# Performance work log

Hardware: AMD Instinct MI355X
Metric: run time of the kernel (lower is better)

Reference implementation:

```python
import jax, jax.numpy as jnp
import numpy as np

DIM_IN = 1024
DIM_OUT = 1024
BATCH = 4
SEQ = 2048


def setup_inputs() -> dict:
    key = jax.random.key(0)
    kx, kq, kk, kv = jax.random.split(key, 4)
    scale = 1.0 / np.sqrt(DIM_IN)
    x = jax.random.normal(kx, (BATCH, SEQ, DIM_IN), dtype=jnp.float32)
    # Weights stored as [dim_in, dim_out] (transpose of torch Linear's [out, in]);
    # y = x @ W is equivalent math to torch's x @ W_t.T
    Wq = jax.random.normal(kq, (DIM_IN, DIM_OUT), dtype=jnp.float32) * scale
    Wk = jax.random.normal(kk, (DIM_IN, DIM_OUT), dtype=jnp.float32) * scale
    Wv = jax.random.normal(kv, (DIM_IN, DIM_OUT), dtype=jnp.float32) * scale
    return {"x": x, "Wq": Wq, "Wk": Wk, "Wv": Wv}


def reference(x, Wq, Wk, Wv):
    # x: [b, s, d_in]; single-head causal self-attention (dropout=0 -> identity)
    q = jnp.einsum("bsd,de->bse", x, Wq)
    k = jnp.einsum("bsd,de->bse", x, Wk)
    v = jnp.einsum("bsd,de->bse", x, Wv)
    dim_k = k.shape[-1]
    scores = jnp.einsum("bqe,bke->bqk", q, k) / jnp.sqrt(jnp.float32(dim_k))
    s = x.shape[1]
    causal = jnp.tril(jnp.ones((s, s), dtype=bool))  # True = keep
    scores = jnp.where(causal[None, :, :], scores, -jnp.inf)
    weights = jax.nn.softmax(scores, axis=-1)
    context = jnp.einsum("bqk,bke->bqe", weights, v)
    return context
```

## Files before the change

kernel.cpp:

```cpp
#include <hip/hip_runtime.h>
#include <cstdint>
#include <cstddef>

typedef unsigned short u16;
typedef __bf16 bf16x8 __attribute__((ext_vector_type(8)));
typedef float f32x4 __attribute__((ext_vector_type(4)));

__device__ inline u16 f2b(float f) {
    uint32_t u = __builtin_bit_cast(uint32_t, f);
    u += 0x7FFFu + ((u >> 16) & 1u);
    return (u16)(u >> 16);
}

__device__ inline void gl2lds16(const u16* g, u16* l) {
    __builtin_amdgcn_global_load_lds(
        (const __attribute__((address_space(1))) void*)g,
        (__attribute__((address_space(3))) void*)l, 16, 0, 0);
}

__global__ void prep_kernel(const float* __restrict__ x, u16* __restrict__ xb,
                            const float* __restrict__ Wq,
                            const float* __restrict__ Wk,
                            const float* __restrict__ Wv,
                            u16* __restrict__ QKWT, u16* __restrict__ WvT) {
    __shared__ u16 t[32][33];
    const int bid = blockIdx.x;
    if (bid < 8192) {
        size_t i = ((size_t)bid * 256 + threadIdx.x) * 4;
        float4 v = *(const float4*)(x + i);
        uint2 pack;
        pack.x = (uint32_t)f2b(v.x) | ((uint32_t)f2b(v.y) << 16);
        pack.y = (uint32_t)f2b(v.z) | ((uint32_t)f2b(v.w) << 16);
        *(uint2*)(xb + i) = pack;
        return;
    }
    const int tb = bid - 8192;
    const int z = tb >> 10;
    const int rem = tb & 1023;
    const int by = (rem >> 5) * 32;
    const int bx = (rem & 31) * 32;
    const float* W = (z == 0) ? Wq : ((z == 1) ? Wk : Wv);
    u16* dst = (z == 0) ? QKWT : ((z == 1) ? QKWT + 1024 * 1024 : WvT);
    const float scale = (z == 0) ? 0.03125f : 1.0f;
    const int tx = threadIdx.x & 31, ty = threadIdx.x >> 5;
    #pragma unroll
    for (int r = 0; r < 32; r += 8)
        t[ty + r][tx] = f2b(W[(size_t)(by + ty + r) * 1024 + bx + tx] * scale);
    __syncthreads();
    #pragma unroll
    for (int r = 0; r < 32; r += 8)
        dst[(size_t)(bx + ty + r) * 1024 + (by + tx)] = t[tx][ty + r];
}

template<int EPI>
__device__ __forceinline__ void gemm_body(
    u16* __restrict__ smem,
    const u16* __restrict__ A, int lda,
    const u16* __restrict__ B, int ldb,
    char* __restrict__ Cb, int ldc,
    int m0, int n0, int Kloc, float* __restrict__ lrow, bool split = false) {
    constexpr int BK = 32;
    const int tid = threadIdx.x;
    const int lane = tid & 63, wave = tid >> 6;
    const int wm = wave >> 1, wn = wave & 1;
    const int fl = lane & 15, fh = lane >> 4;

    const int q0 = wave * 2;
    const int srow = lane >> 2;
    const int skoff = ((lane & 3) ^ ((lane >> 3) & 3)) * 8;
    const u16* ApL0 = A + (size_t)(m0 + q0 * 16 + srow) * lda + skoff;
    const u16* ApL1 = ApL0 + (size_t)16 * lda;
    const u16* BpL0 = B + (size_t)(n0 + q0 * 16 + srow) * ldb + skoff;
    const u16* BpL1 = BpL0 + (size_t)16 * ldb;

    u16* const Ab[2] = { smem, smem + 4096 };
    u16* const Bb[2] = { smem + 8192, smem + 12288 };

    auto issue = [&](int buf, int k0) {
        gl2lds16(ApL0 + k0, Ab[buf] + q0 * 512);
        gl2lds16(ApL1 + k0, Ab[buf] + q0 * 512 + 512);
        gl2lds16(BpL0 + k0, Bb[buf] + q0 * 512);
        gl2lds16(BpL1 + k0, Bb[buf] + q0 * 512 + 512);
    };

    const f32x4 vzero = {0.f, 0.f, 0.f, 0.f};
    f32x4 acc[4][4];
    #pragma unroll
    for (int i = 0; i < 4; ++i)
        #pragma unroll
        for (int j = 0; j < 4; ++j) acc[i][j] = vzero;

    const int rcx = (fl >> 1) & 3;

    issue(0, 0);
    int buf = 0;
    for (int k0 = 0; k0 < Kloc; k0 += BK, buf ^= 1) {
        __syncthreads();
        if (k0 + BK < Kloc) issue(buf ^ 1, k0 + BK);
        bf16x8 af[4], bfr[4];
        #pragma unroll
        for (int t = 0; t < 4; ++t) {
            af[t]  = *(const bf16x8*)&Ab[buf][(wm * 64 + t * 16 + fl) * BK + (fh ^ rcx) * 8];
            bfr[t] = *(const bf16x8*)&Bb[buf][(wn * 64 + t * 16 + fl) * BK + (fh ^ rcx) * 8];
        }
        #pragma unroll
        for (int mt = 0; mt < 4; ++mt)
            #pragma unroll
            for (int nt = 0; nt < 4; ++nt)
                acc[mt][nt] = __builtin_amdgcn_mfma_f32_16x16x32_bf16(
                    af[mt], bfr[nt], acc[mt][nt], 0, 0, 0);
    }

    if (EPI == 0) {
        u16* Cp = (u16*)Cb;
        #pragma unroll
        for (int mt = 0; mt < 4; ++mt)
            #pragma unroll
            for (int nt = 0; nt < 4; ++nt)
                #pragma unroll
                for (int r = 0; r < 4; ++r) {
                    int row = m0 + wm * 64 + mt * 16 + fh * 4 + r;
                    int col = n0 + wn * 64 + nt * 16 + fl;
                    Cp[(size_t)row * ldc + col] = f2b(acc[mt][nt][r]);
                }
    } else if (EPI == 2) {
        u16* Cp = (u16*)Cb;
        #pragma unroll
        for (int mt = 0; mt < 4; ++mt)
            #pragma unroll
            for (int r = 0; r < 4; ++r) {
                int row = m0 + wm * 64 + mt * 16 + fh * 4 + r;
                float part = 0.f;
                #pragma unroll
                for (int nt = 0; nt < 4; ++nt) {
                    int col = n0 + wn * 64 + nt * 16 + fl;
                    float p = (col <= row) ? __expf(acc[mt][nt][r]) : 0.f;
                    part += p;
                    Cp[(size_t)row * ldc + col] = f2b(p);
                }
                #pragma unroll
                for (int off = 1; off < 16; off <<= 1)
                    part += __shfl_xor(part, off, 64);
                if (fl == 0) atomicAdd(lrow + row, part);
            }
    } else {
        float* Cp = (float*)Cb;
        #pragma unroll
        for (int mt = 0; mt < 4; ++mt)
            #pragma unroll
            for (int r = 0; r < 4; ++r) {
                int row = m0 + wm * 64 + mt * 16 + fh * 4 + r;
                float inv = 1.0f / lrow[row];
                #pragma unroll
                for (int nt = 0; nt < 4; ++nt) {
                    int col = n0 + wn * 64 + nt * 16 + fl;
                    float v = acc[mt][nt][r] * inv;
                    if (split) atomicAdd(&Cp[(size_t)row * ldc + col], v);
                    else       Cp[(size_t)row * ldc + col] = v;
                }
            }
    }
}

__global__ __launch_bounds__(256)
void proj_kernel(const u16* __restrict__ xb, const u16* __restrict__ QKWT,
                 const u16* __restrict__ WvT, u16* __restrict__ QK,
                 u16* __restrict__ Vt) {
    __shared__ __align__(16) u16 smem[16384];
    int bid = blockIdx.x;
    if (bid < 1024) {
        int jt = bid & 15, it = bid >> 4;
        gemm_body<0>(smem, xb, 1024, QKWT, 1024, (char*)QK, 2048,
                     it * 128, jt * 128, 1024, nullptr);
    } else {
        int b = bid - 1024;
        int jt = b & 63, it = b >> 6;
        gemm_body<0>(smem, WvT, 1024, xb, 1024, (char*)Vt, 8192,
                     it * 128, jt * 128, 1024, nullptr);
    }
}

__global__ __launch_bounds__(256)
void scores_kernel(const u16* __restrict__ QK, u16* __restrict__ P,
                   float* __restrict__ l) {
    __shared__ __align__(16) u16 smem[16384];
    const int t = blockIdx.x, z = blockIdx.y;
    int it = (int)((sqrtf(8.0f * t + 1.0f) - 1.0f) * 0.5f);
    while ((it + 1) * (it + 2) / 2 <= t) ++it;
    while (it * (it + 1) / 2 > t) --it;
    const int jt = t - it * (it + 1) / 2;
    const u16* Qz = QK + (size_t)z * 2048 * 2048;
    const u16* Kz = Qz + 1024;
    u16* Pz = P + (size_t)z * 2048 * 2048;
    gemm_body<2>(smem, Qz, 2048, Kz, 2048, (char*)Pz, 2048,
                 it * 128, jt * 128, 1024, l + (size_t)z * 2048);
}

__global__ __launch_bounds__(256)
void out_kernel(const u16* __restrict__ P, const u16* __restrict__ Vt,
                float* __restrict__ out, float* __restrict__ l) {
    __shared__ __align__(16) u16 smem[16384];
    const int jt = blockIdx.x, c = blockIdx.y, z = blockIdx.z;
    int it, k0, kloc;
    bool split;
    if (c < 16) {
        it = 8 + (c >> 1);
        kloc = (it + 1) * 64;
        k0 = (c & 1) * kloc;
        split = true;
    } else {
        it = c - 16;
        k0 = 0;
        kloc = (it + 1) * 128;
        split = false;
    }
    gemm_body<3>(smem, P + (size_t)z * 2048 * 2048 + k0, 2048,
                 Vt + (size_t)z * 2048 + k0, 8192,
                 (char*)(out + (size_t)z * 2048 * 1024), 1024,
                 it * 128, jt * 128, kloc, l + (size_t)z * 2048, split);
}

extern "C" void kernel_launch(void* const* d_in, const int* in_sizes, int n_in,
                              void* d_out, int out_size, void* d_ws, size_t ws_size,
                              hipStream_t stream) {
    (void)in_sizes; (void)n_in; (void)ws_size;
    const float* x  = (const float*)d_in[0];
    const float* Wq = (const float*)d_in[1];
    const float* Wk = (const float*)d_in[2];
    const float* Wv = (const float*)d_in[3];
    float* out = (float*)d_out;

    const size_t MB = 1u << 20;
    char* ws = (char*)d_ws;
    u16* xb   = (u16*)(ws);
    u16* QKWT = (u16*)(ws + 16 * MB);
    u16* WvT  = (u16*)(ws + 20 * MB);
    u16* QK   = (u16*)(ws + 22 * MB);
    u16* Vt   = (u16*)(ws + 54 * MB);
    u16* P    = (u16*)(ws + 70 * MB);
    float* l  = (float*)(ws + 102 * MB);

    hipMemsetAsync(l, 0, 8192 * sizeof(float), stream);
    hipMemsetAsync(out, 0, (size_t)out_size * sizeof(float), stream);
    prep_kernel<<<8192 + 3072, 256, 0, stream>>>(x, xb, Wq, Wk, Wv, QKWT, WvT);

    proj_kernel<<<1536, 256, 0, stream>>>(xb, QKWT, WvT, QK, Vt);
    scores_kernel<<<dim3(136, 4), 256, 0, stream>>>(QK, P, l);
    out_kernel<<<dim3(8, 24, 4), 256, 0, stream>>>(P, Vt, out, l);
}
```

Measured before the change: 266.1 us.

## Fuse memsets into prep kernel, rebalance causal split-K, drop LDS swizzle

Zeroing of the output and the row-sum buffer moves into extra work in prep_kernel, which removes two memset launches. The P·V kernel is re-partitioned into uniform 512-wide K chunks per causal row tile, giving 40 chunks per column tile, and batch is folded into the x grid dimension to even out work across blocks. The XOR swizzle on LDS tile addressing is removed, which simplifies the index math but may reintroduce LDS bank conflicts in the MFMA fragment loads. More blocks now take the atomic split path.

After: 289.7 us. +8.9%, slower.

```diff
diff --git a/kernel.cpp b/kernel.cpp
--- a/kernel.cpp
+++ b/kernel.cpp
@@ -22,7 +22,8 @@
                             const float* __restrict__ Wq,
                             const float* __restrict__ Wk,
                             const float* __restrict__ Wv,
-                            u16* __restrict__ QKWT, u16* __restrict__ WvT) {
+                            u16* __restrict__ QKWT, u16* __restrict__ WvT,
+                            float* __restrict__ out, float* __restrict__ l) {
     __shared__ u16 t[32][33];
     const int bid = blockIdx.x;
     if (bid < 8192) {
@@ -32,6 +33,12 @@
         pack.x = (uint32_t)f2b(v.x) | ((uint32_t)f2b(v.y) << 16);
         pack.y = (uint32_t)f2b(v.z) | ((uint32_t)f2b(v.w) << 16);
         *(uint2*)(xb + i) = pack;
+        *(float4*)(out + i) = make_float4(0.f, 0.f, 0.f, 0.f);
+        return;
+    }
+    if (bid >= 11264) {
+        size_t i = ((size_t)(bid - 11264) * 256 + threadIdx.x) * 4;
+        *(float4*)(l + i) = make_float4(0.f, 0.f, 0.f, 0.f);
         return;
     }
     const int tb = bid - 8192;
@@ -66,8 +73,7 @@
     const int fl = lane & 15, fh = lane >> 4;
 
     const int q0 = wave * 2;
-    const int srow = lane >> 2;
-    const int skoff = ((lane & 3) ^ ((lane >> 3) & 3)) * 8;
+    const int srow = lane >> 2, skoff = (lane & 3) * 8;
     const u16* ApL0 = A + (size_t)(m0 + q0 * 16 + srow) * lda + skoff;
     const u16* ApL1 = ApL0 + (size_t)16 * lda;
     const u16* BpL0 = B + (size_t)(n0 + q0 * 16 + srow) * ldb + skoff;
@@ -90,8 +96,6 @@
         #pragma unroll
         for (int j = 0; j < 4; ++j) acc[i][j] = vzero;
 
-    const int rcx = (fl >> 1) & 3;
-
     issue(0, 0);
     int buf = 0;
     for (int k0 = 0; k0 < Kloc; k0 += BK, buf ^= 1) {
@@ -100,8 +104,8 @@
         bf16x8 af[4], bfr[4];
         #pragma unroll
         for (int t = 0; t < 4; ++t) {
-            af[t]  = *(const bf16x8*)&Ab[buf][(wm * 64 + t * 16 + fl) * BK + (fh ^ rcx) * 8];
-            bfr[t] = *(const bf16x8*)&Bb[buf][(wn * 64 + t * 16 + fl) * BK + (fh ^ rcx) * 8];
+            af[t]  = *(const bf16x8*)&Ab[buf][(wm * 64 + t * 16 + fl) * BK + fh * 8];
+            bfr[t] = *(const bf16x8*)&Bb[buf][(wn * 64 + t * 16 + fl) * BK + fh * 8];
         }
         #pragma unroll
         for (int mt = 0; mt < 4; ++mt)
@@ -200,20 +204,17 @@
 void out_kernel(const u16* __restrict__ P, const u16* __restrict__ Vt,
                 float* __restrict__ out, float* __restrict__ l) {
     __shared__ __align__(16) u16 smem[16384];
-    const int jt = blockIdx.x, c = blockIdx.y, z = blockIdx.z;
-    int it, k0, kloc;
-    bool split;
-    if (c < 16) {
-        it = 8 + (c >> 1);
-        kloc = (it + 1) * 64;
-        k0 = (c & 1) * kloc;
-        split = true;
-    } else {
-        it = c - 16;
-        k0 = 0;
-        kloc = (it + 1) * 128;
-        split = false;
-    }
+    const int jt = blockIdx.x & 7, z = blockIdx.x >> 3;
+    int c = blockIdx.y, it = 15;
+    for (int i = 15; i >= 0; --i) {
+        int n = (i >> 2) + 1;
+        if (c < n) { it = i; break; }
+        c -= n;
+    }
+    const int Ktot = (it + 1) * 128;
+    const int k0 = c * 512;
+    const int kloc = min(512, Ktot - k0);
+    const bool split = (Ktot > 512);
     gemm_body<3>(smem, P + (size_t)z * 2048 * 2048 + k0, 2048,
                  Vt + (size_t)z * 2048 + k0, 8192,
                  (char*)(out + (size_t)z * 2048 * 1024), 1024,
@@ -223,7 +224,7 @@
 extern "C" void kernel_launch(void* const* d_in, const int* in_sizes, int n_in,
                               void* d_out, int out_size, void* d_ws, size_t ws_size,
                               hipStream_t stream) {
-    (void)in_sizes; (void)n_in; (void)ws_size;
+    (void)in_sizes; (void)n_in; (void)out_size; (void)ws_size;
     const float* x  = (const float*)d_in[0];
     const float* Wq = (const float*)d_in[1];
     const float* Wk = (const float*)d_in[2];
@@ -240,11 +241,8 @@
     u16* P    = (u16*)(ws + 70 * MB);
     float* l  = (float*)(ws + 102 * MB);
 
-    hipMemsetAsync(l, 0, 8192 * sizeof(float), stream);
-    hipMemsetAsync(out, 0, (size_t)out_size * sizeof(float), stream);
-    prep_kernel<<<8192 + 3072, 256, 0, stream>>>(x, xb, Wq, Wk, Wv, QKWT, WvT);
-
+    prep_kernel<<<8192 + 3072 + 8, 256, 0, stream>>>(x, xb, Wq, Wk, Wv, QKWT, WvT, out, l);
     proj_kernel<<<1536, 256, 0, stream>>>(xb, QKWT, WvT, QK, Vt);
     scores_kernel<<<dim3(136, 4), 256, 0, stream>>>(QK, P, l);
-    out_kernel<<<dim3(8, 24, 4), 256, 0, stream>>>(P, Vt, out, l);
-}
+    out_kernel<<<dim3(32, 40), 256, 0, stream>>>(P, Vt, out, l);
+}
```
